# Performance work log

Hardware: AMD Instinct MI355X
Metric: run time of the kernel (lower is better)

## Reference

```python
import jax, jax.numpy as jnp
import numpy as np

N = 100000   # nodes
E = 2500000  # edges (before self-loops)
G = 64       # graphs in the batch


def _glorot(key, fi, fo):
    return jax.random.normal(key, (fi, fo), jnp.float32) * jnp.sqrt(2.0 / (fi + fo))


def setup_inputs() -> dict:
    key = jax.random.key(0)
    ks = jax.random.split(key, 8)
    x = jax.random.normal(ks[0], (N, 3), jnp.float32)
    edge_index = jax.random.randint(ks[1], (2, E), 0, N)
    batch = jnp.sort(jax.random.randint(ks[2], (N,), 0, G))
    return dict(
        x=x, edge_index=edge_index, batch=batch,
        W1=_glorot(ks[3], 3, 16),  b1=jnp.zeros((16,), jnp.float32),
        W2=_glorot(ks[4], 16, 32), b2=jnp.zeros((32,), jnp.float32),
        W3=_glorot(ks[5], 32, 16), b3=jnp.zeros((16,), jnp.float32),
        W4=_glorot(ks[6], 16, 2),  b4=jnp.zeros((2,), jnp.float32),
    )


def reference(x, edge_index, batch, W1, b1, W2, b2, W3, b3, W4, b4):
    # PyG GCNConv: add self-loops, sym-normalize by deg^{-1/2}, gather->scatter-add.
    loops = jnp.arange(N)
    src = jnp.concatenate([edge_index[0], loops])  # [E+N]
    dst = jnp.concatenate([edge_index[1], loops])
    deg = jax.ops.segment_sum(jnp.ones_like(dst, jnp.float32), dst, num_segments=N)
    dinv = jax.lax.rsqrt(jnp.maximum(deg, 1.0))  # deg >= 1 due to self-loops
    norm = (dinv[src] * dinv[dst])[:, None]      # [E+N, 1]

    def gcn_conv(h, W, b):
        h = h @ W                                  # [N, out]
        msg = h[src] * norm                        # gather + edge scaling
        agg = jax.ops.segment_sum(msg, dst, num_segments=N)  # scatter-add
        return agg + b

    h = jax.nn.relu(gcn_conv(x, W1, b1))
    h = jax.nn.relu(gcn_conv(h, W2, b2))
    h = jax.nn.relu(gcn_conv(h, W3, b3))
    # F.dropout with training=False (module in eval) is identity
    h = gcn_conv(h, W4, b4)                        # [N, 2]

    # global_mean_pool over graph ids
    sums = jax.ops.segment_sum(h, batch, num_segments=G)
    cnts = jax.ops.segment_sum(jnp.ones((N,), h.dtype), batch, num_segments=G)
    pooled = sums / jnp.maximum(cnts, 1.0)[:, None]  # [G, 2]
    return jax.nn.log_softmax(pooled, axis=1)
```

## Files before the change

### kernel.cpp

```cpp
#include <hip/hip_runtime.h>
#include <hip/hip_fp16.h>
#include <cmath>

static constexpr int NN = 100000;
static constexpr int NE = 2500000;
static constexpr int NG = 64;
static constexpr int NBUCK = (NN + 255) / 256;
static constexpr int CHUNK = 4096;
static constexpr int NCHUNK = (NE + CHUNK - 1) / CHUNK;
static constexpr int CAP = 8192;

union H8 { float4 f4; __half2 h2[4]; };
union H4 { float2 f2; __half2 h2[2]; };

__device__ inline void unpack_add(float* a, float4 r) {
    H8 u; u.f4 = r;
#pragma unroll
    for (int k = 0; k < 4; ++k) { float2 f = __half22float2(u.h2[k]); a[2*k] += f.x; a[2*k+1] += f.y; }
}
__device__ inline float2 pack4(const float* f) {
    H4 u;
    u.h2[0] = __floats2half2_rn(f[0], f[1]);
    u.h2[1] = __floats2half2_rn(f[2], f[3]);
    return u.f2;
}

__global__ void p1_hist(const int* __restrict__ dst, int* __restrict__ Ht) {
    __shared__ int hist[NBUCK];
    int t = threadIdx.x, c = blockIdx.x;
    for (int i = t; i < NBUCK; i += 256) hist[i] = 0;
    __syncthreads();
    int e0 = c * CHUNK, e1 = min(e0 + CHUNK, NE);
    for (int e = e0 + t; e < e1; e += 256) atomicAdd(&hist[dst[e] >> 8], 1);
    __syncthreads();
    for (int b = t; b < NBUCK; b += 256) Ht[(size_t)b * NCHUNK + c] = hist[b];
}

__global__ void p2_scan(int* __restrict__ Ht, int* __restrict__ count,
                        float* __restrict__ pooled3) {
    __shared__ int s[256];
    int b = blockIdx.x, t = threadIdx.x;
    if (b == 0 && t < NG * 3) pooled3[t] = 0.0f;
    int* row = Ht + (size_t)b * NCHUNK;
    int carry = 0;
    for (int seg = 0; seg < 3; ++seg) {
        int idx = seg * 256 + t;
        int v = (idx < NCHUNK) ? row[idx] : 0;
        __syncthreads();
        s[t] = v;
        __syncthreads();
#pragma unroll
        for (int off = 1; off < 256; off <<= 1) {
            int y = (t >= off) ? s[t - off] : 0;
            __syncthreads();
            s[t] += y;
            __syncthreads();
        }
        int incl = s[t];
        int segtot = s[255];
        if (idx < NCHUNK) row[idx] = incl - v + carry;
        carry += segtot;
    }
    if (t == 0) count[b] = carry;
}

__global__ void p3_scatter(const int* __restrict__ src, const int* __restrict__ dst,
                           const int* __restrict__ Ht, int* __restrict__ staging) {
    __shared__ int cur[NBUCK];
    int t = threadIdx.x, bid = blockIdx.x;
    int x = bid & 7, o = bid >> 3;
    int len = 76 + (x < 3 ? 1 : 0);
    if (o >= len) return;
    int c = x * 76 + min(x, 3) + o;
    for (int b = t; b < NBUCK; b += 256) cur[b] = Ht[(size_t)b * NCHUNK + c];
    __syncthreads();
    int e0 = c * CHUNK, e1 = min(e0 + CHUNK, NE);
    for (int e = e0 + t; e < e1; e += 256) {
        int d = dst[e];
        int b = d >> 8;
        int r = atomicAdd(&cur[b], 1);
        staging[((size_t)b << 13) + r] = src[e] | ((d & 255) << 17);
    }
}

__global__ void csr_build_kernel(const int* __restrict__ staging, const int* __restrict__ count,
                                 int* __restrict__ deg_i, float* __restrict__ dinv,
                                 int* __restrict__ row_start, int* __restrict__ csr_src) {
    __shared__ int hist[256];
    __shared__ int scn[256];
    __shared__ int cur[256];
    int b = blockIdx.x, t = threadIdx.x;
    int cnt = count[b];
    int base = b << 13;
    hist[t] = 0;
    __syncthreads();
    const int* st = staging + ((size_t)b << 13);
    for (int i = t; i < cnt; i += 256) atomicAdd(&hist[st[i] >> 17], 1);
    __syncthreads();
    int h = hist[t];
    scn[t] = h; __syncthreads();
#pragma unroll
    for (int off = 1; off < 256; off <<= 1) {
        int y = (t >= off) ? scn[t - off] : 0;
        __syncthreads();
        scn[t] += y;
        __syncthreads();
    }
    int ex = scn[t] - h;
    int v = (b << 8) + t;
    if (v < NN) {
        deg_i[v]     = h;
        row_start[v] = base + ex;
        dinv[v]      = rsqrtf((float)h + 1.0f);
    }
    cur[t] = ex;
    __syncthreads();
    for (int i = t; i < cnt; i += 256) {
        int p = st[i];
        int r = atomicAdd(&cur[p >> 17], 1);
        csr_src[base + r] = p & 0x1FFFF;
    }
}

__global__ void xs4_kernel(const float* __restrict__ x, const float* __restrict__ dinv,
                           float4* __restrict__ xs4) {
    int v = blockIdx.x * 256 + threadIdx.x;
    if (v < NN) {
        float dv = dinv[v];
        xs4[v] = make_float4(x[v * 3] * dv, x[v * 3 + 1] * dv, x[v * 3 + 2] * dv, 0.0f);
    }
}

__global__ void __launch_bounds__(256) agg3t1_kernel(const float4* __restrict__ xs4,
        const int* __restrict__ csr, const int* __restrict__ rs, const int* __restrict__ deg,
        const float* __restrict__ dinv, const float* __restrict__ W1,
        const float* __restrict__ b1, float2* __restrict__ g2h) {
    __shared__ float sW1[48], sb1[16];
    int t = threadIdx.x;
    if (t < 48) sW1[t] = W1[t];
    if (t < 16) sb1[t] = b1[t];
    __syncthreads();
    int tid = blockIdx.x * 256 + t;
    int v = tid >> 2, p = tid & 3;
    if (v >= NN) return;
    float a0 = 0.0f, a1 = 0.0f, a2 = 0.0f;
    if (p == 0) { float4 s = xs4[v]; a0 = s.x; a1 = s.y; a2 = s.z; }
    int s0 = rs[v], cnt = deg[v];
    for (int j = p; j < cnt; j += 4) {
        float4 q = xs4[csr[s0 + j]];
        a0 += q.x; a1 += q.y; a2 += q.z;
    }
    a0 += __shfl_xor(a0, 1); a1 += __shfl_xor(a1, 1); a2 += __shfl_xor(a2, 1);
    a0 += __shfl_xor(a0, 2); a1 += __shfl_xor(a1, 2); a2 += __shfl_xor(a2, 2);
    float dv = dinv[v];
    a0 *= dv; a1 *= dv; a2 *= dv;
    float f[4];
#pragma unroll
    for (int k = 0; k < 4; ++k) {
        int fo = p * 4 + k;
        float g = fmaf(a0, sW1[fo], fmaf(a1, sW1[16 + fo], fmaf(a2, sW1[32 + fo], sb1[fo])));
        f[k] = fmaxf(g, 0.0f) * dv;
    }
    g2h[v * 4 + p] = pack4(f);
}

__global__ void __launch_bounds__(256) agg16mid_kernel(const float4* __restrict__ g2h,
        const int* __restrict__ csr, const int* __restrict__ rs, const int* __restrict__ deg,
        const float* __restrict__ dinv, const float* __restrict__ W2,
        const float* __restrict__ b2, const float* __restrict__ W3,
        float2* __restrict__ g3h) {
    __shared__ float sW2[512], sW3[512], sb2[32];
    int t = threadIdx.x;
    for (int i = t; i < 512; i += 256) { sW2[i] = W2[i]; sW3[i] = W3[i]; }
    if (t < 32) sb2[t] = b2[t];
    __syncthreads();
    int tid = blockIdx.x * 256 + t;
    int v = tid >> 2, p = tid & 3;
    if (v >= NN) return;
    float a[16];
#pragma unroll
    for (int f = 0; f < 16; ++f) a[f] = 0.0f;
    if (p == 0) { unpack_add(a, g2h[v * 2]); unpack_add(a + 8, g2h[v * 2 + 1]); }
    int s0 = rs[v], cnt = deg[v];
    for (int j = p; j < cnt; j += 4) {
        int s = csr[s0 + j];
        unpack_add(a,     g2h[s * 2]);
        unpack_add(a + 8, g2h[s * 2 + 1]);
    }
#pragma unroll
    for (int f = 0; f < 16; ++f) a[f] += __shfl_xor(a[f], 1);
#pragma unroll
    for (int f = 0; f < 16; ++f) a[f] += __shfl_xor(a[f], 2);
    float dv = dinv[v];
#pragma unroll
    for (int f = 0; f < 16; ++f) a[f] *= dv;
    float h2[32];
#pragma unroll
    for (int fo = 0; fo < 32; ++fo) {
        float s = sb2[fo];
#pragma unroll
        for (int fi = 0; fi < 16; ++fi) s = fmaf(a[fi], sW2[fi * 32 + fo], s);
        h2[fo] = fmaxf(s, 0.0f);
    }
    float o[4];
#pragma unroll
    for (int k = 0; k < 4; ++k) {
        int fo = p * 4 + k;
        float s = 0.0f;
#pragma unroll
        for (int fi = 0; fi < 32; ++fi) s = fmaf(h2[fi], sW3[fi * 16 + fo], s);
        o[k] = s * dv;
    }
    g3h[v * 4 + p] = pack4(o);
}

__global__ void __launch_bounds__(256) agg16t4_kernel(const float4* __restrict__ g3h,
        const int* __restrict__ csr, const int* __restrict__ rs, const int* __restrict__ deg,
        const float* __restrict__ dinv, const float* __restrict__ b3,
        const float* __restrict__ W4, float2* __restrict__ g4) {
    __shared__ float sb3[16], sW4[32];
    int t = threadIdx.x;
    if (t < 16) sb3[t] = b3[t];
    if (t < 32) sW4[t] = W4[t];
    __syncthreads();
    int tid = blockIdx.x * 256 + t;
    int v = tid >> 2, p = tid & 3;
    if (v >= NN) return;
    float a[16];
#pragma unroll
    for (int f = 0; f < 16; ++f) a[f] = 0.0f;
    if (p == 0) { unpack_add(a, g3h[v * 2]); unpack_add(a + 8, g3h[v * 2 + 1]); }
    int s0 = rs[v], cnt = deg[v];
    for (int j = p; j < cnt; j += 4) {
        int s = csr[s0 + j];
        unpack_add(a,     g3h[s * 2]);
        unpack_add(a + 8, g3h[s * 2 + 1]);
    }
#pragma unroll
    for (int f = 0; f < 16; ++f) a[f] += __shfl_xor(a[f], 1);
#pragma unroll
    for (int f = 0; f < 16; ++f) a[f] += __shfl_xor(a[f], 2);
    if (p != 0) return;
    float dv = dinv[v];
    float o0 = 0.0f, o1 = 0.0f;
#pragma unroll
    for (int f = 0; f < 16; ++f) {
        float h3 = fmaxf(fmaf(a[f], dv, sb3[f]), 0.0f);
        o0 = fmaf(h3, sW4[f * 2 + 0], o0);
        o1 = fmaf(h3, sW4[f * 2 + 1], o1);
    }
    g4[v] = make_float2(o0 * dv, o1 * dv);
}

__global__ void __launch_bounds__(256) agg2pool_kernel(const float2* __restrict__ g4,
        const int* __restrict__ csr, const int* __restrict__ rs, const int* __restrict__ deg,
        const float* __restrict__ dinv, const float* __restrict__ b4,
        const int* __restrict__ batch, float* __restrict__ pooled3) {
    __shared__ float spool[NG * 3];
    int t = threadIdx.x;
    for (int i = t; i < NG * 3; i += 256) spool[i] = 0.0f;
    __syncthreads();
    int tid = blockIdx.x * 256 + t;
    int v = tid >> 2, p = tid & 3;
    if (v < NN) {
        float a0 = 0.0f, a1 = 0.0f;
        if (p == 0) { float2 s = g4[v]; a0 = s.x; a1 = s.y; }
        int s0 = rs[v], cnt = deg[v];
        for (int j = p; j < cnt; j += 4) {
            float2 q = g4[csr[s0 + j]];
            a0 += q.x; a1 += q.y;
        }
        a0 += __shfl_xor(a0, 1); a1 += __shfl_xor(a1, 1);
        a0 += __shfl_xor(a0, 2); a1 += __shfl_xor(a1, 2);
        if (p == 0) {
            float dv = dinv[v];
            float o0 = fmaf(a0, dv, b4[0]);
            float o1 = fmaf(a1, dv, b4[1]);
            int gi = batch[v];
            atomicAdd(&spool[gi * 3 + 0], o0);
            atomicAdd(&spool[gi * 3 + 1], o1);
            atomicAdd(&spool[gi * 3 + 2], 1.0f);
        }
    }
    __syncthreads();
    for (int i = t; i < NG * 3; i += 256)
        if (spool[i] != 0.0f) atomicAdd(&pooled3[i], spool[i]);
}

__global__ void lsm_kernel(const float* __restrict__ pooled3, float* __restrict__ out) {
    int g = threadIdx.x;
    if (g < NG) {
        float c = fmaxf(pooled3[g * 3 + 2], 1.0f);
        float a = pooled3[g * 3 + 0] / c;
        float b = pooled3[g * 3 + 1] / c;
        float m = fmaxf(a, b);
        float lse = m + logf(expf(a - m) + expf(b - m));
        out[g * 2 + 0] = a - lse;
        out[g * 2 + 1] = b - lse;
    }
}

extern "C" void kernel_launch(void* const* d_in, const int* in_sizes, int n_in,
                              void* d_out, int out_size, void* d_ws, size_t ws_size,
                              hipStream_t stream) {
    (void)in_sizes; (void)n_in; (void)out_size; (void)ws_size;

    const float* x   = (const float*)d_in[0];
    const int*   ei  = (const int*)d_in[1];
    const int*   bat = (const int*)d_in[2];
    const float* W1  = (const float*)d_in[3];
    const float* b1  = (const float*)d_in[4];
    const float* W2  = (const float*)d_in[5];
    const float* b2  = (const float*)d_in[6];
    const float* W3  = (const float*)d_in[7];
    const float* b3  = (const float*)d_in[8];
    const float* W4  = (const float*)d_in[9];
    const float* b4  = (const float*)d_in[10];
    float* out = (float*)d_out;

    const int* src = ei;
    const int* dst = ei + NE;

    char* w = (char*)d_ws;
    int*    Ht        = (int*)w;    w += ((size_t)NBUCK * NCHUNK * 4 + 15) & ~15ull;
    int*    count     = (int*)w;    w += ((size_t)NBUCK * 4 + 15) & ~15ull;
    int*    staging   = (int*)w;    w += (size_t)NBUCK * CAP * 4;
    int*    csr_src   = (int*)w;    w += (size_t)NBUCK * CAP * 4;
    int*    deg_i     = (int*)w;    w += (size_t)NN * 4;
    int*    row_start = (int*)w;    w += (size_t)NN * 4;
    float*  dinv      = (float*)w;  w += (size_t)NN * 4;
    float4* xs4       = (float4*)w; w += (size_t)NN * 16;
    float*  g2h       = (float*)w;  w += (size_t)NN * 32;
    float*  g3h       = (float*)w;  w += (size_t)NN * 32;
    float2* g4        = (float2*)w; w += (size_t)NN * 8;
    float*  pooled3   = (float*)w;  w += NG * 3 * 4;

    const int gN4 = (NN * 4 + 255) / 256;

    p1_hist<<<NCHUNK, 256, 0, stream>>>(dst, Ht);
    p2_scan<<<NBUCK, 256, 0, stream>>>(Ht, count, pooled3);
    p3_scatter<<<616, 256, 0, stream>>>(src, dst, Ht, staging);
    csr_build_kernel<<<NBUCK, 256, 0, stream>>>(staging, count, deg_i, dinv, row_start, csr_src);

    xs4_kernel<<<NBUCK, 256, 0, stream>>>(x, dinv, xs4);

    agg3t1_kernel<<<gN4, 256, 0, stream>>>(xs4, csr_src, row_start, deg_i, dinv, W1, b1,
                                           (float2*)g2h);
    agg16mid_kernel<<<gN4, 256, 0, stream>>>((const float4*)g2h, csr_src, row_start, deg_i,
                                             dinv, W2, b2, W3, (float2*)g3h);
    agg16t4_kernel<<<gN4, 256, 0, stream>>>((const float4*)g3h, csr_src, row_start, deg_i,
                                            dinv, b3, W4, g4);
    agg2pool_kernel<<<gN4, 256, 0, stream>>>(g4, csr_src, row_start, deg_i, dinv, b4, bat,
                                             pooled3);

    lsm_kernel<<<1, 64, 0, stream>>>(pooled3, out);
}
```

Baseline: 157.0 us.

## Split 16-wide aggregation by feature slice per lane and fuse xs into CSR build

The 16-feature aggregation kernels now give each of the 4 lanes per node its own 4-feature fp16 slice (8 bytes) and have every lane walk all neighbors, replacing the edge-split scheme that read 32 bytes per edge per lane and reduced 16 values through shuffles. The layer-1 input is stored as packed fp16 (8 bytes instead of a 16-byte float4) and is produced inside csr_build, which removes the separate xs4 kernel launch. Each lane's gather is narrower, but every lane now loops over the full degree and reads the CSR index stream four times per node. fp16 storage of the scaled input adds rounding error.

```diff
diff --git a/kernel.cpp b/kernel.cpp
--- a/kernel.cpp
+++ b/kernel.cpp
@@ -10,14 +10,8 @@
 static constexpr int NCHUNK = (NE + CHUNK - 1) / CHUNK;
 static constexpr int CAP = 8192;
 
-union H8 { float4 f4; __half2 h2[4]; };
 union H4 { float2 f2; __half2 h2[2]; };
 
-__device__ inline void unpack_add(float* a, float4 r) {
-    H8 u; u.f4 = r;
-#pragma unroll
-    for (int k = 0; k < 4; ++k) { float2 f = __half22float2(u.h2[k]); a[2*k] += f.x; a[2*k+1] += f.y; }
-}
 __device__ inline float2 pack4(const float* f) {
     H4 u;
     u.h2[0] = __floats2half2_rn(f[0], f[1]);
@@ -84,8 +78,10 @@
 }
 
 __global__ void csr_build_kernel(const int* __restrict__ staging, const int* __restrict__ count,
+                                 const float* __restrict__ x,
                                  int* __restrict__ deg_i, float* __restrict__ dinv,
-                                 int* __restrict__ row_start, int* __restrict__ csr_src) {
+                                 int* __restrict__ row_start, int* __restrict__ csr_src,
+                                 float2* __restrict__ xsh) {
     __shared__ int hist[256];
     __shared__ int scn[256];
     __shared__ int cur[256];
@@ -109,9 +105,14 @@
     int ex = scn[t] - h;
     int v = (b << 8) + t;
     if (v < NN) {
+        float dv = rsqrtf((float)h + 1.0f);
         deg_i[v]     = h;
         row_start[v] = base + ex;
-        dinv[v]      = rsqrtf((float)h + 1.0f);
+        dinv[v]      = dv;
+        H4 u;
+        u.h2[0] = __floats2half2_rn(x[v * 3] * dv, x[v * 3 + 1] * dv);
+        u.h2[1] = __floats2half2_rn(x[v * 3 + 2] * dv, 0.0f);
+        xsh[v] = u.f2;
     }
     cur[t] = ex;
     __syncthreads();
@@ -122,16 +123,7 @@
     }
 }
 
-__global__ void xs4_kernel(const float* __restrict__ x, const float* __restrict__ dinv,
-                           float4* __restrict__ xs4) {
-    int v = blockIdx.x * 256 + threadIdx.x;
-    if (v < NN) {
-        float dv = dinv[v];
-        xs4[v] = make_float4(x[v * 3] * dv, x[v * 3 + 1] * dv, x[v * 3 + 2] * dv, 0.0f);
-    }
-}
-
-__global__ void __launch_bounds__(256) agg3t1_kernel(const float4* __restrict__ xs4,
+__global__ void __launch_bounds__(256) agg3t1_kernel(const float2* __restrict__ xsh,
         const int* __restrict__ csr, const int* __restrict__ rs, const int* __restrict__ deg,
         const float* __restrict__ dinv, const float* __restrict__ W1,
         const float* __restrict__ b1, float2* __restrict__ g2h) {
@@ -144,11 +136,16 @@
     int v = tid >> 2, p = tid & 3;
     if (v >= NN) return;
     float a0 = 0.0f, a1 = 0.0f, a2 = 0.0f;
-    if (p == 0) { float4 s = xs4[v]; a0 = s.x; a1 = s.y; a2 = s.z; }
+    if (p == 0) {
+        H4 u; u.f2 = xsh[v];
+        float2 f0 = __half22float2(u.h2[0]), f1 = __half22float2(u.h2[1]);
+        a0 = f0.x; a1 = f0.y; a2 = f1.x;
+    }
     int s0 = rs[v], cnt = deg[v];
     for (int j = p; j < cnt; j += 4) {
-        float4 q = xs4[csr[s0 + j]];
-        a0 += q.x; a1 += q.y; a2 += q.z;
+        H4 u; u.f2 = xsh[csr[s0 + j]];
+        float2 f0 = __half22float2(u.h2[0]), f1 = __half22float2(u.h2[1]);
+        a0 += f0.x; a1 += f0.y; a2 += f1.x;
     }
     a0 += __shfl_xor(a0, 1); a1 += __shfl_xor(a1, 1); a2 += __shfl_xor(a2, 1);
     a0 += __shfl_xor(a0, 2); a1 += __shfl_xor(a1, 2); a2 += __shfl_xor(a2, 2);
@@ -164,7 +161,7 @@
     g2h[v * 4 + p] = pack4(f);
 }
 
-__global__ void __launch_bounds__(256) agg16mid_kernel(const float4* __restrict__ g2h,
+__global__ void __launch_bounds__(256) agg16mid_kernel(const float2* __restrict__ g2h,
         const int* __restrict__ csr, const int* __restrict__ rs, const int* __restrict__ deg,
         const float* __restrict__ dinv, const float* __restrict__ W2,
         const float* __restrict__ b2, const float* __restrict__ W3,
@@ -177,23 +174,30 @@
     int tid = blockIdx.x * 256 + t;
     int v = tid >> 2, p = tid & 3;
     if (v >= NN) return;
+    float q0, q1, q2, q3;
+    {
+        H4 u; u.f2 = g2h[v * 4 + p];
+        float2 f0 = __half22float2(u.h2[0]), f1 = __half22float2(u.h2[1]);
+        q0 = f0.x; q1 = f0.y; q2 = f1.x; q3 = f1.y;
+    }
+    int s0 = rs[v], cnt = deg[v];
+    for (int j = 0; j < cnt; ++j) {
+        int s = csr[s0 + j];
+        H4 u; u.f2 = g2h[s * 4 + p];
+        float2 f0 = __half22float2(u.h2[0]), f1 = __half22float2(u.h2[1]);
+        q0 += f0.x; q1 += f0.y; q2 += f1.x; q3 += f1.y;
+    }
+    float dv = dinv[v];
+    q0 *= dv; q1 *= dv; q2 *= dv; q3 *= dv;
+    int lane = t & 63, gb = lane & ~3;
     float a[16];
 #pragma unroll
-    for (int f = 0; f < 16; ++f) a[f] = 0.0f;
-    if (p == 0) { unpack_add(a, g2h[v * 2]); unpack_add(a + 8, g2h[v * 2 + 1]); }
-    int s0 = rs[v], cnt = deg[v];
-    for (int j = p; j < cnt; j += 4) {
-        int s = csr[s0 + j];
-        unpack_add(a,     g2h[s * 2]);
-        unpack_add(a + 8, g2h[s * 2 + 1]);
-    }
-#pragma unroll
-    for (int f = 0; f < 16; ++f) a[f] += __shfl_xor(a[f], 1);
-#pragma unroll
-    for (int f = 0; f < 16; ++f) a[f] += __shfl_xor(a[f], 2);
-    float dv = dinv[v];
-#pragma unroll
-    for (int f = 0; f < 16; ++f) a[f] *= dv;
+    for (int q = 0; q < 4; ++q) {
+        a[q * 4 + 0] = __shfl(q0, gb + q);
+        a[q * 4 + 1] = __shfl(q1, gb + q);
+        a[q * 4 + 2] = __shfl(q2, gb + q);
+        a[q * 4 + 3] = __shfl(q3, gb + q);
+    }
     float h2[32];
 #pragma unroll
     for (int fo = 0; fo < 32; ++fo) {
@@ -214,7 +218,7 @@
     g3h[v * 4 + p] = pack4(o);
 }
 
-__global__ void __launch_bounds__(256) agg16t4_kernel(const float4* __restrict__ g3h,
+__global__ void __launch_bounds__(256) agg16t4_kernel(const float2* __restrict__ g3h,
         const int* __restrict__ csr, const int* __restrict__ rs, const int* __restrict__ deg,
         const float* __restrict__ dinv, const float* __restrict__ b3,
         const float* __restrict__ W4, float2* __restrict__ g4) {
@@ -226,30 +230,31 @@
     int tid = blockIdx.x * 256 + t;
     int v = tid >> 2, p = tid & 3;
     if (v >= NN) return;
-    float a[16];
-#pragma unroll
-    for (int f = 0; f < 16; ++f) a[f] = 0.0f;
-    if (p == 0) { unpack_add(a, g3h[v * 2]); unpack_add(a + 8, g3h[v * 2 + 1]); }
+    float q[4];
+    {
+        H4 u; u.f2 = g3h[v * 4 + p];
+        float2 f0 = __half22float2(u.h2[0]), f1 = __half22float2(u.h2[1]);
+        q[0] = f0.x; q[1] = f0.y; q[2] = f1.x; q[3] = f1.y;
+    }
     int s0 = rs[v], cnt = deg[v];
-    for (int j = p; j < cnt; j += 4) {
+    for (int j = 0; j < cnt; ++j) {
         int s = csr[s0 + j];
-        unpack_add(a,     g3h[s * 2]);
-        unpack_add(a + 8, g3h[s * 2 + 1]);
-    }
-#pragma unroll
-    for (int f = 0; f < 16; ++f) a[f] += __shfl_xor(a[f], 1);
-#pragma unroll
-    for (int f = 0; f < 16; ++f) a[f] += __shfl_xor(a[f], 2);
-    if (p != 0) return;
+        H4 u; u.f2 = g3h[s * 4 + p];
+        float2 f0 = __half22float2(u.h2[0]), f1 = __half22float2(u.h2[1]);
+        q[0] += f0.x; q[1] += f0.y; q[2] += f1.x; q[3] += f1.y;
+    }
     float dv = dinv[v];
     float o0 = 0.0f, o1 = 0.0f;
 #pragma unroll
-    for (int f = 0; f < 16; ++f) {
-        float h3 = fmaxf(fmaf(a[f], dv, sb3[f]), 0.0f);
+    for (int k = 0; k < 4; ++k) {
+        int f = p * 4 + k;
+        float h3 = fmaxf(fmaf(q[k], dv, sb3[f]), 0.0f);
         o0 = fmaf(h3, sW4[f * 2 + 0], o0);
         o1 = fmaf(h3, sW4[f * 2 + 1], o1);
     }
-    g4[v] = make_float2(o0 * dv, o1 * dv);
+    o0 += __shfl_xor(o0, 1); o1 += __shfl_xor(o1, 1);
+    o0 += __shfl_xor(o0, 2); o1 += __shfl_xor(o1, 2);
+    if (p == 0) g4[v] = make_float2(o0 * dv, o1 * dv);
 }
 
 __global__ void __launch_bounds__(256) agg2pool_kernel(const float2* __restrict__ g4,
@@ -329,9 +334,9 @@
     int*    deg_i     = (int*)w;    w += (size_t)NN * 4;
     int*    row_start = (int*)w;    w += (size_t)NN * 4;
     float*  dinv      = (float*)w;  w += (size_t)NN * 4;
-    float4* xs4       = (float4*)w; w += (size_t)NN * 16;
-    float*  g2h       = (float*)w;  w += (size_t)NN * 32;
-    float*  g3h       = (float*)w;  w += (size_t)NN * 32;
+    float2* xsh       = (float2*)w; w += (size_t)NN * 8;
+    float2* g2h       = (float2*)w; w += (size_t)NN * 32;
+    float2* g3h       = (float2*)w; w += (size_t)NN * 32;
     float2* g4        = (float2*)w; w += (size_t)NN * 8;
     float*  pooled3   = (float*)w;  w += NG * 3 * 4;
 
@@ -340,16 +345,13 @@
     p1_hist<<<NCHUNK, 256, 0, stream>>>(dst, Ht);
     p2_scan<<<NBUCK, 256, 0, stream>>>(Ht, count, pooled3);
     p3_scatter<<<616, 256, 0, stream>>>(src, dst, Ht, staging);
-    csr_build_kernel<<<NBUCK, 256, 0, stream>>>(staging, count, deg_i, dinv, row_start, csr_src);
-
-    xs4_kernel<<<NBUCK, 256, 0, stream>>>(x, dinv, xs4);
-
-    agg3t1_kernel<<<gN4, 256, 0, stream>>>(xs4, csr_src, row_start, deg_i, dinv, W1, b1,
-                                           (float2*)g2h);
-    agg16mid_kernel<<<gN4, 256, 0, stream>>>((const float4*)g2h, csr_src, row_start, deg_i,
-                                             dinv, W2, b2, W3, (float2*)g3h);
-    agg16t4_kernel<<<gN4, 256, 0, stream>>>((const float4*)g3h, csr_src, row_start, deg_i,
-                                            dinv, b3, W4, g4);
+    csr_build_kernel<<<NBUCK, 256, 0, stream>>>(staging, count, x, deg_i, dinv, row_start,
+                                                csr_src, xsh);
+
+    agg3t1_kernel<<<gN4, 256, 0, stream>>>(xsh, csr_src, row_start, deg_i, dinv, W1, b1, g2h);
+    agg16mid_kernel<<<gN4, 256, 0, stream>>>(g2h, csr_src, row_start, deg_i, dinv, W2, b2, W3,
+                                             g3h);
+    agg16t4_kernel<<<gN4, 256, 0, stream>>>(g3h, csr_src, row_start, deg_i, dinv, b3, W4, g4);
     agg2pool_kernel<<<gN4, 256, 0, stream>>>(g4, csr_src, row_start, deg_i, dinv, b4, bat,
                                              pooled3);
 
```

New measurement: 173.6 us. +10.5%, slower.

## Use 8 lanes per node in aggregation kernels, fuse xs4 into CSR build, store half-precision input

Applied to the files above, without the earlier changes.

Each of the four gather/aggregate kernels now assigns 8 threads per destination node instead of 4, adding one more shuffle-reduction step and having each lane emit two fp16 outputs. The separate xs4 kernel is folded into the CSR build kernel, which writes the dinv-scaled input features packed as fp16 (8 bytes per node instead of a 16-byte float4). The goal is more memory-level parallelism for the irregular gathers (average degree about 26), one less launch, and less gather traffic in layer one. The cost is more threads and shuffles per node, plus extra fp16 rounding on the input features.

```diff
diff --git a/kernel.cpp b/kernel.cpp
--- a/kernel.cpp
+++ b/kernel.cpp
@@ -18,11 +18,9 @@
 #pragma unroll
     for (int k = 0; k < 4; ++k) { float2 f = __half22float2(u.h2[k]); a[2*k] += f.x; a[2*k+1] += f.y; }
 }
-__device__ inline float2 pack4(const float* f) {
-    H4 u;
-    u.h2[0] = __floats2half2_rn(f[0], f[1]);
-    u.h2[1] = __floats2half2_rn(f[2], f[3]);
-    return u.f2;
+__device__ inline unsigned pack2(float f0, float f1) {
+    __half2 h = __floats2half2_rn(f0, f1);
+    return *reinterpret_cast<unsigned*>(&h);
 }
 
 __global__ void p1_hist(const int* __restrict__ dst, int* __restrict__ Ht) {
@@ -84,8 +82,10 @@
 }
 
 __global__ void csr_build_kernel(const int* __restrict__ staging, const int* __restrict__ count,
+                                 const float* __restrict__ x,
                                  int* __restrict__ deg_i, float* __restrict__ dinv,
-                                 int* __restrict__ row_start, int* __restrict__ csr_src) {
+                                 int* __restrict__ row_start, int* __restrict__ csr_src,
+                                 float2* __restrict__ xsh) {
     __shared__ int hist[256];
     __shared__ int scn[256];
     __shared__ int cur[256];
@@ -109,9 +109,14 @@
     int ex = scn[t] - h;
     int v = (b << 8) + t;
     if (v < NN) {
+        float dv = rsqrtf((float)h + 1.0f);
         deg_i[v]     = h;
         row_start[v] = base + ex;
-        dinv[v]      = rsqrtf((float)h + 1.0f);
+        dinv[v]      = dv;
+        H4 u;
+        u.h2[0] = __floats2half2_rn(x[v * 3] * dv, x[v * 3 + 1] * dv);
+        u.h2[1] = __floats2half2_rn(x[v * 3 + 2] * dv, 0.0f);
+        xsh[v] = u.f2;
     }
     cur[t] = ex;
     __syncthreads();
@@ -122,67 +127,64 @@
     }
 }
 
-__global__ void xs4_kernel(const float* __restrict__ x, const float* __restrict__ dinv,
-                           float4* __restrict__ xs4) {
-    int v = blockIdx.x * 256 + threadIdx.x;
-    if (v < NN) {
-        float dv = dinv[v];
-        xs4[v] = make_float4(x[v * 3] * dv, x[v * 3 + 1] * dv, x[v * 3 + 2] * dv, 0.0f);
-    }
-}
-
-__global__ void __launch_bounds__(256) agg3t1_kernel(const float4* __restrict__ xs4,
+__global__ void __launch_bounds__(256) agg3t1_kernel(const float2* __restrict__ xsh,
         const int* __restrict__ csr, const int* __restrict__ rs, const int* __restrict__ deg,
         const float* __restrict__ dinv, const float* __restrict__ W1,
-        const float* __restrict__ b1, float2* __restrict__ g2h) {
+        const float* __restrict__ b1, unsigned* __restrict__ g2h) {
     __shared__ float sW1[48], sb1[16];
     int t = threadIdx.x;
     if (t < 48) sW1[t] = W1[t];
     if (t < 16) sb1[t] = b1[t];
     __syncthreads();
     int tid = blockIdx.x * 256 + t;
-    int v = tid >> 2, p = tid & 3;
+    int v = tid >> 3, p = tid & 7;
     if (v >= NN) return;
     float a0 = 0.0f, a1 = 0.0f, a2 = 0.0f;
-    if (p == 0) { float4 s = xs4[v]; a0 = s.x; a1 = s.y; a2 = s.z; }
+    if (p == 0) {
+        H4 u; u.f2 = xsh[v];
+        float2 f0 = __half22float2(u.h2[0]), f1 = __half22float2(u.h2[1]);
+        a0 = f0.x; a1 = f0.y; a2 = f1.x;
+    }
     int s0 = rs[v], cnt = deg[v];
-    for (int j = p; j < cnt; j += 4) {
-        float4 q = xs4[csr[s0 + j]];
-        a0 += q.x; a1 += q.y; a2 += q.z;
+    for (int j = p; j < cnt; j += 8) {
+        H4 u; u.f2 = xsh[csr[s0 + j]];
+        float2 f0 = __half22float2(u.h2[0]), f1 = __half22float2(u.h2[1]);
+        a0 += f0.x; a1 += f0.y; a2 += f1.x;
     }
     a0 += __shfl_xor(a0, 1); a1 += __shfl_xor(a1, 1); a2 += __shfl_xor(a2, 1);
     a0 += __shfl_xor(a0, 2); a1 += __shfl_xor(a1, 2); a2 += __shfl_xor(a2, 2);
+    a0 += __shfl_xor(a0, 4); a1 += __shfl_xor(a1, 4); a2 += __shfl_xor(a2, 4);
     float dv = dinv[v];
     a0 *= dv; a1 *= dv; a2 *= dv;
-    float f[4];
-#pragma unroll
-    for (int k = 0; k < 4; ++k) {
-        int fo = p * 4 + k;
+    float f[2];
+#pragma unroll
+    for (int k = 0; k < 2; ++k) {
+        int fo = p * 2 + k;
         float g = fmaf(a0, sW1[fo], fmaf(a1, sW1[16 + fo], fmaf(a2, sW1[32 + fo], sb1[fo])));
         f[k] = fmaxf(g, 0.0f) * dv;
     }
-    g2h[v * 4 + p] = pack4(f);
+    g2h[v * 8 + p] = pack2(f[0], f[1]);
 }
 
 __global__ void __launch_bounds__(256) agg16mid_kernel(const float4* __restrict__ g2h,
         const int* __restrict__ csr, const int* __restrict__ rs, const int* __restrict__ deg,
         const float* __restrict__ dinv, const float* __restrict__ W2,
         const float* __restrict__ b2, const float* __restrict__ W3,
-        float2* __restrict__ g3h) {
+        unsigned* __restrict__ g3h) {
     __shared__ float sW2[512], sW3[512], sb2[32];
     int t = threadIdx.x;
     for (int i = t; i < 512; i += 256) { sW2[i] = W2[i]; sW3[i] = W3[i]; }
     if (t < 32) sb2[t] = b2[t];
     __syncthreads();
     int tid = blockIdx.x * 256 + t;
-    int v = tid >> 2, p = tid & 3;
+    int v = tid >> 3, p = tid & 7;
     if (v >= NN) return;
     float a[16];
 #pragma unroll
     for (int f = 0; f < 16; ++f) a[f] = 0.0f;
     if (p == 0) { unpack_add(a, g2h[v * 2]); unpack_add(a + 8, g2h[v * 2 + 1]); }
     int s0 = rs[v], cnt = deg[v];
-    for (int j = p; j < cnt; j += 4) {
+    for (int j = p; j < cnt; j += 8) {
         int s = csr[s0 + j];
         unpack_add(a,     g2h[s * 2]);
         unpack_add(a + 8, g2h[s * 2 + 1]);
@@ -191,6 +193,8 @@
     for (int f = 0; f < 16; ++f) a[f] += __shfl_xor(a[f], 1);
 #pragma unroll
     for (int f = 0; f < 16; ++f) a[f] += __shfl_xor(a[f], 2);
+#pragma unroll
+    for (int f = 0; f < 16; ++f) a[f] += __shfl_xor(a[f], 4);
     float dv = dinv[v];
 #pragma unroll
     for (int f = 0; f < 16; ++f) a[f] *= dv;
@@ -202,16 +206,16 @@
         for (int fi = 0; fi < 16; ++fi) s = fmaf(a[fi], sW2[fi * 32 + fo], s);
         h2[fo] = fmaxf(s, 0.0f);
     }
-    float o[4];
-#pragma unroll
-    for (int k = 0; k < 4; ++k) {
-        int fo = p * 4 + k;
+    float o[2];
+#pragma unroll
+    for (int k = 0; k < 2; ++k) {
+        int fo = p * 2 + k;
         float s = 0.0f;
 #pragma unroll
         for (int fi = 0; fi < 32; ++fi) s = fmaf(h2[fi], sW3[fi * 16 + fo], s);
         o[k] = s * dv;
     }
-    g3h[v * 4 + p] = pack4(o);
+    g3h[v * 8 + p] = pack2(o[0], o[1]);
 }
 
 __global__ void __launch_bounds__(256) agg16t4_kernel(const float4* __restrict__ g3h,
@@ -224,14 +228,14 @@
     if (t < 32) sW4[t] = W4[t];
     __syncthreads();
     int tid = blockIdx.x * 256 + t;
-    int v = tid >> 2, p = tid & 3;
+    int v = tid >> 3, p = tid & 7;
     if (v >= NN) return;
     float a[16];
 #pragma unroll
     for (int f = 0; f < 16; ++f) a[f] = 0.0f;
     if (p == 0) { unpack_add(a, g3h[v * 2]); unpack_add(a + 8, g3h[v * 2 + 1]); }
     int s0 = rs[v], cnt = deg[v];
-    for (int j = p; j < cnt; j += 4) {
+    for (int j = p; j < cnt; j += 8) {
         int s = csr[s0 + j];
         unpack_add(a,     g3h[s * 2]);
         unpack_add(a + 8, g3h[s * 2 + 1]);
@@ -240,6 +244,8 @@
     for (int f = 0; f < 16; ++f) a[f] += __shfl_xor(a[f], 1);
 #pragma unroll
     for (int f = 0; f < 16; ++f) a[f] += __shfl_xor(a[f], 2);
+#pragma unroll
+    for (int f = 0; f < 16; ++f) a[f] += __shfl_xor(a[f], 4);
     if (p != 0) return;
     float dv = dinv[v];
     float o0 = 0.0f, o1 = 0.0f;
@@ -261,17 +267,18 @@
     for (int i = t; i < NG * 3; i += 256) spool[i] = 0.0f;
     __syncthreads();
     int tid = blockIdx.x * 256 + t;
-    int v = tid >> 2, p = tid & 3;
+    int v = tid >> 3, p = tid & 7;
     if (v < NN) {
         float a0 = 0.0f, a1 = 0.0f;
         if (p == 0) { float2 s = g4[v]; a0 = s.x; a1 = s.y; }
         int s0 = rs[v], cnt = deg[v];
-        for (int j = p; j < cnt; j += 4) {
+        for (int j = p; j < cnt; j += 8) {
             float2 q = g4[csr[s0 + j]];
             a0 += q.x; a1 += q.y;
         }
         a0 += __shfl_xor(a0, 1); a1 += __shfl_xor(a1, 1);
         a0 += __shfl_xor(a0, 2); a1 += __shfl_xor(a1, 2);
+        a0 += __shfl_xor(a0, 4); a1 += __shfl_xor(a1, 4);
         if (p == 0) {
             float dv = dinv[v];
             float o0 = fmaf(a0, dv, b4[0]);
@@ -322,35 +329,33 @@
     const int* dst = ei + NE;
 
     char* w = (char*)d_ws;
-    int*    Ht        = (int*)w;    w += ((size_t)NBUCK * NCHUNK * 4 + 15) & ~15ull;
-    int*    count     = (int*)w;    w += ((size_t)NBUCK * 4 + 15) & ~15ull;
-    int*    staging   = (int*)w;    w += (size_t)NBUCK * CAP * 4;
-    int*    csr_src   = (int*)w;    w += (size_t)NBUCK * CAP * 4;
-    int*    deg_i     = (int*)w;    w += (size_t)NN * 4;
-    int*    row_start = (int*)w;    w += (size_t)NN * 4;
-    float*  dinv      = (float*)w;  w += (size_t)NN * 4;
-    float4* xs4       = (float4*)w; w += (size_t)NN * 16;
-    float*  g2h       = (float*)w;  w += (size_t)NN * 32;
-    float*  g3h       = (float*)w;  w += (size_t)NN * 32;
-    float2* g4        = (float2*)w; w += (size_t)NN * 8;
-    float*  pooled3   = (float*)w;  w += NG * 3 * 4;
-
-    const int gN4 = (NN * 4 + 255) / 256;
+    int*      Ht        = (int*)w;      w += ((size_t)NBUCK * NCHUNK * 4 + 15) & ~15ull;
+    int*      count     = (int*)w;      w += ((size_t)NBUCK * 4 + 15) & ~15ull;
+    int*      staging   = (int*)w;      w += (size_t)NBUCK * CAP * 4;
+    int*      csr_src   = (int*)w;      w += (size_t)NBUCK * CAP * 4;
+    int*      deg_i     = (int*)w;      w += (size_t)NN * 4;
+    int*      row_start = (int*)w;      w += (size_t)NN * 4;
+    float*    dinv      = (float*)w;    w += (size_t)NN * 4;
+    float2*   xsh       = (float2*)w;   w += (size_t)NN * 8;
+    unsigned* g2h       = (unsigned*)w; w += (size_t)NN * 32;
+    unsigned* g3h       = (unsigned*)w; w += (size_t)NN * 32;
+    float2*   g4        = (float2*)w;   w += (size_t)NN * 8;
+    float*    pooled3   = (float*)w;    w += NG * 3 * 4;
+
+    const int gN8 = (NN * 8 + 255) / 256;
 
     p1_hist<<<NCHUNK, 256, 0, stream>>>(dst, Ht);
     p2_scan<<<NBUCK, 256, 0, stream>>>(Ht, count, pooled3);
     p3_scatter<<<616, 256, 0, stream>>>(src, dst, Ht, staging);
-    csr_build_kernel<<<NBUCK, 256, 0, stream>>>(staging, count, deg_i, dinv, row_start, csr_src);
-
-    xs4_kernel<<<NBUCK, 256, 0, stream>>>(x, dinv, xs4);
-
-    agg3t1_kernel<<<gN4, 256, 0, stream>>>(xs4, csr_src, row_start, deg_i, dinv, W1, b1,
-                                           (float2*)g2h);
-    agg16mid_kernel<<<gN4, 256, 0, stream>>>((const float4*)g2h, csr_src, row_start, deg_i,
-                                             dinv, W2, b2, W3, (float2*)g3h);
-    agg16t4_kernel<<<gN4, 256, 0, stream>>>((const float4*)g3h, csr_src, row_start, deg_i,
+    csr_build_kernel<<<NBUCK, 256, 0, stream>>>(staging, count, x, deg_i, dinv, row_start,
+                                                csr_src, xsh);
+
+    agg3t1_kernel<<<gN8, 256, 0, stream>>>(xsh, csr_src, row_start, deg_i, dinv, W1, b1, g2h);
+    agg16mid_kernel<<<gN8, 256, 0, stream>>>((const float4*)g2h, csr_src, row_start, deg_i,
+                                             dinv, W2, b2, W3, g3h);
+    agg16t4_kernel<<<gN8, 256, 0, stream>>>((const float4*)g3h, csr_src, row_start, deg_i,
                                             dinv, b3, W4, g4);
-    agg2pool_kernel<<<gN4, 256, 0, stream>>>(g4, csr_src, row_start, deg_i, dinv, b4, bat,
+    agg2pool_kernel<<<gN8, 256, 0, stream>>>(g4, csr_src, row_start, deg_i, dinv, b4, bat,
                                              pooled3);
 
     lsm_kernel<<<1, 64, 0, stream>>>(pooled3, out);
```

After: 158.2 us. Within noise of the previous version (+0.8%).
